# Optimization experiments

Hardware: AMD Instinct MI355X
Metric: run time of the kernel (lower is better)

Reference implementation:

```python
import jax, jax.numpy as jnp
import numpy as np

B, N, DI, DS, DP, DM, S = 64, 4096, 64, 64, 64, 128, 7
NUM_ITER = 3
EPS_ATTN = 1e-8
LN_EPS = 1e-5


def setup_inputs() -> dict:
    key = jax.random.key(0)
    ks = jax.random.split(key, 12)
    rn = lambda k, shp, sc=1.0: (jax.random.normal(k, shp, jnp.float32) * sc)
    return {
        "x": rn(ks[0], (B, N, DI)),
        "ln_inp_g": jnp.ones((DI,), jnp.float32),
        "ln_inp_b": jnp.zeros((DI,), jnp.float32),
        "ln_slot_g": jnp.ones((DS,), jnp.float32),
        "ln_slot_b": jnp.zeros((DS,), jnp.float32),
        "slots_init": rn(ks[1], (1, S, DS)),
        "Wk": rn(ks[2], (DI, DP), 1.0 / np.sqrt(DI)),
        "Wv": rn(ks[3], (DI, DP), 1.0 / np.sqrt(DI)),
        "Wq": rn(ks[4], (DS, DP), 1.0 / np.sqrt(DS)),
        "gru_wih": rn(ks[5], (3 * DS, DP), 1.0 / np.sqrt(DS)),
        "gru_whh": rn(ks[6], (3 * DS, DS), 1.0 / np.sqrt(DS)),
        "gru_bih": jnp.zeros((3 * DS,), jnp.float32),
        "gru_bhh": jnp.zeros((3 * DS,), jnp.float32),
        "mlp_w1": rn(ks[7], (DS, DM), 1.0 / np.sqrt(DS)),
        "mlp_b1": jnp.zeros((DM,), jnp.float32),
        "mlp_w2": rn(ks[8], (DM, DS), 1.0 / np.sqrt(DM)),
        "mlp_b2": jnp.zeros((DS,), jnp.float32),
    }


def _layernorm(x, g, b):
    m = jnp.mean(x, axis=-1, keepdims=True)
    v = jnp.mean(jnp.square(x - m), axis=-1, keepdims=True)
    return (x - m) * jax.lax.rsqrt(v + LN_EPS) * g + b


def _gru_cell(u, h, wih, whh, bih, bhh):
    # PyTorch GRUCell semantics
    gi = u @ wih.T + bih  # [*, 3*DS]
    gh = h @ whh.T + bhh
    ir, iz, inn = jnp.split(gi, 3, axis=-1)
    hr, hz, hn = jnp.split(gh, 3, axis=-1)
    r = jax.nn.sigmoid(ir + hr)
    z = jax.nn.sigmoid(iz + hz)
    n = jnp.tanh(inn + r * hn)
    return (1.0 - z) * n + z * h


def reference(x, ln_inp_g, ln_inp_b, ln_slot_g, ln_slot_b, slots_init,
              Wk, Wv, Wq, gru_wih, gru_whh, gru_bih, gru_bhh,
              mlp_w1, mlp_b1, mlp_w2, mlp_b2):
    x = _layernorm(x, ln_inp_g, ln_inp_b)          # [B,N,DI]
    k = x @ Wk                                      # [B,N,DP] (hoisted; x fixed across iters)
    v = x @ Wv                                      # [B,N,DP]
    slots = jnp.broadcast_to(slots_init, (x.shape[0], S, DS))
    scale = 1.0 / np.sqrt(DP)
    for _ in range(NUM_ITER):
        slots_prev = slots
        sn = _layernorm(slots, ln_slot_g, ln_slot_b)
        q = sn @ Wq                                 # [B,S,DP]
        attn = jnp.einsum('bnd,bsd->bns', k, q) * scale
        attn = jax.nn.softmax(attn, axis=-1) + EPS_ATTN      # softmax over slots
        weights = attn / jnp.sum(attn, axis=1, keepdims=True)  # normalize over N
        updates = jnp.einsum('bns,bnd->bsd', weights, v)     # [B,S,DP]
        h = _gru_cell(updates.reshape(-1, DP), slots_prev.reshape(-1, DS),
                      gru_wih, gru_whh, gru_bih, gru_bhh)
        slots = h.reshape(-1, S, DS)
        slots = slots + (jax.nn.relu(slots @ mlp_w1 + mlp_b1) @ mlp_w2 + mlp_b2)
    return slots
```

## Files before the change

kernel.cpp:

```cpp
#include <hip/hip_runtime.h>
#include <stdint.h>

#define L2E 1.44269504088896f

static __device__ __forceinline__ float wsum(float v) {
    #pragma unroll
    for (int m = 1; m < 64; m <<= 1) v += __shfl_xor(v, m, 64);
    return v;
}
static __device__ __forceinline__ float sigm(float x) {
    return 1.0f / (1.0f + __builtin_amdgcn_exp2f(-x * L2E));
}
static __device__ __forceinline__ float tanh_(float x) {
    const float ax = fabsf(x);
    const float t = __builtin_amdgcn_exp2f(-2.0f * ax * L2E);
    const float r = (1.0f - t) / (1.0f + t);
    return (x < 0.f) ? -r : r;
}

template <int CTRL>
static __device__ __forceinline__ float dppterm(float v) {
    return __int_as_float(__builtin_amdgcn_update_dpp(
        0, __float_as_int(v), CTRL, 0xF, 0xF, true));
}
static __device__ __forceinline__ float red8(float v) {
    v += dppterm<0xB1>(v);
    v += dppterm<0x4E>(v);
    v += dppterm<0x141>(v);
    return v;
}

__global__ __launch_bounds__(256) void init_kernel(
    const float* __restrict__ s0,
    const float* __restrict__ lsg, const float* __restrict__ lsb,
    const float* __restrict__ Wq,  const float* __restrict__ Wk,
    const float* __restrict__ lig, const float* __restrict__ lib,
    const float* __restrict__ wih, const float* __restrict__ whh,
    float* __restrict__ slots, float* __restrict__ gkq, float* __restrict__ aux,
    float* __restrict__ wihT, float* __restrict__ whhT, float* __restrict__ WkT)
{
    __shared__ float wkT[4096];
    __shared__ float scr[4][64];
    const int tid = threadIdx.x, lane = tid & 63, wv = tid >> 6;
    const int idx = blockIdx.x * 256 + tid;

    if (idx < 12288) {
        const int i = idx / 192, j = idx - i * 192;
        wihT[idx] = wih[j * 64 + i];
    } else if (idx < 24576) {
        const int o = idx - 12288;
        const int i = o / 192, j = o - i * 192;
        whhT[o] = whh[j * 64 + i];
    } else {
        const int o = idx - 24576;
        const int p = o >> 6, d = o & 63;
        WkT[o] = Wk[d * 64 + p];
    }

    const int r = blockIdx.x * 4 + wv;
    const int s = r % 7;
    #pragma unroll
    for (int i = tid; i < 4096; i += 256) {
        const int d = i >> 6, p = i & 63;
        wkT[p * 64 + d] = Wk[i];
    }
    const float h = s0[s * 64 + lane];
    slots[r * 64 + lane] = h;
    __syncthreads();

    const float mean = wsum(h) * (1.0f / 64.0f);
    const float d = h - mean;
    const float var = wsum(d * d) * (1.0f / 64.0f);
    const float rs = rsqrtf(var + 1e-5f);
    const float sn = d * rs * lsg[lane] + lsb[lane];
    scr[wv][lane] = sn;
    __syncthreads();
    float q = 0.f;
    #pragma unroll 8
    for (int i = 0; i < 64; ++i) q = fmaf(scr[wv][i], Wq[i * 64 + lane], q);
    q *= 0.125f;
    __syncthreads();
    scr[wv][lane] = q;
    __syncthreads();
    float kq = 0.f;
    #pragma unroll 8
    for (int p = 0; p < 64; ++p) kq = fmaf(wkT[p * 64 + lane], scr[wv][p], kq);
    const float bk = wsum(lib[lane] * kq);
    const float gk = lig[lane] * kq;
    const float g1 = wsum(gk);
    gkq[r * 64 + lane] = gk;
    if (lane == 0) { aux[r * 2] = g1; aux[r * 2 + 1] = bk; }
}

__global__ __launch_bounds__(256, 2) void attn_kernel(
    const float* __restrict__ x,
    const float* __restrict__ gkq, const float* __restrict__ aux,
    float* __restrict__ Ypart)
{
    __shared__ float ybuf[16][460];
    const int tid = threadIdx.x, lane = tid & 63, wv = tid >> 6;
    const int b = blockIdx.x >> 4, chunk16 = blockIdx.x & 15;
    const int ck  = lane & 7;
    const int rsl = lane >> 3;

    float gk[7][8];
    {
        const float4* gp = (const float4*)(gkq + b * 448 + ck * 8);
        #pragma unroll
        for (int s = 0; s < 7; ++s) {
            const float4 u0 = gp[s * 16], u1 = gp[s * 16 + 1];
            gk[s][0] = u0.x; gk[s][1] = u0.y; gk[s][2] = u0.z; gk[s][3] = u0.w;
            gk[s][4] = u1.x; gk[s][5] = u1.y; gk[s][6] = u1.z; gk[s][7] = u1.w;
        }
    }
    const float* ab = aux + b * 14;
    float g1[7], bk[7];
    #pragma unroll
    for (int s = 0; s < 7; ++s) { g1[s] = ab[2 * s]; bk[s] = ab[2 * s + 1]; }

    float Yacc[7][8];
    #pragma unroll
    for (int s = 0; s < 7; ++s)
        #pragma unroll
        for (int j = 0; j < 8; ++j) Yacc[s][j] = 0.f;
    float cacc[7] = {0.f, 0.f, 0.f, 0.f, 0.f, 0.f, 0.f};

    const float* rb = x + (((long)b * 4096) + chunk16 * 256 + wv * 64 + rsl) * 64
                        + ck * 8;
    float4 a0 = *(const float4*)(rb);
    float4 a1 = *(const float4*)(rb + 4);
    #pragma unroll 1
    for (int g = 0; g < 8; ++g) {
        const int gn = (g < 7) ? g + 1 : 7;
        const float4 b0 = *(const float4*)(rb + gn * 512);
        const float4 b1 = *(const float4*)(rb + gn * 512 + 4);

        const float xv[8] = {a0.x, a0.y, a0.z, a0.w, a1.x, a1.y, a1.z, a1.w};
        float sum = 0.f, ss = 0.f;
        #pragma unroll
        for (int j = 0; j < 8; ++j) { sum += xv[j]; ss = fmaf(xv[j], xv[j], ss); }
        float acc[7];
        #pragma unroll
        for (int s = 0; s < 7; ++s) {
            float a = 0.f;
            #pragma unroll
            for (int j = 0; j < 8; ++j) a = fmaf(xv[j], gk[s][j], a);
            acc[s] = a;
        }
        sum = red8(sum);
        ss  = red8(ss);
        #pragma unroll
        for (int s = 0; s < 7; ++s) acc[s] = red8(acc[s]);

        const float m   = sum * (1.0f / 64.0f);
        const float var = ss * (1.0f / 64.0f) - m * m;
        const float rs  = rsqrtf(var + 1e-5f);
        const float rsm = rs * m;
        float t[7];
        #pragma unroll
        for (int s = 0; s < 7; ++s)
            t[s] = fmaf(rs, acc[s], fmaf(-rsm, g1[s], bk[s]));
        float mx = t[0];
        #pragma unroll
        for (int s = 1; s < 7; ++s) mx = fmaxf(mx, t[s]);
        float e[7], se = 0.f;
        #pragma unroll
        for (int s = 0; s < 7; ++s) {
            e[s] = __builtin_amdgcn_exp2f((t[s] - mx) * L2E);
            se += e[s];
        }
        const float inv = 1.0f / se;
        #pragma unroll
        for (int s = 0; s < 7; ++s) {
            const float w = fmaf(e[s], inv, 1e-8f);
            cacc[s] += w;
            const float wrs = w * rs;
            #pragma unroll
            for (int j = 0; j < 8; ++j)
                Yacc[s][j] = fmaf(wrs, xv[j], Yacc[s][j]);
        }
        a0 = b0; a1 = b1;
    }

    #pragma unroll
    for (int s = 0; s < 7; ++s) {
        #pragma unroll
        for (int j = 0; j < 8; ++j)
            Yacc[s][j] += dppterm<0x128>(Yacc[s][j]);
        cacc[s] += dppterm<0x128>(cacc[s]);
    }
    if (((lane >> 3) & 1) == 0) {
        const int sub = lane >> 4;
        float* yb = &ybuf[wv * 4 + sub][ck * 8];
        #pragma unroll
        for (int s = 0; s < 7; ++s) {
            #pragma unroll
            for (int j = 0; j < 8; ++j) yb[s * 64 + j] = Yacc[s][j];
        }
        if (ck == 0) {
            #pragma unroll
            for (int s = 0; s < 7; ++s)
                ybuf[wv * 4 + sub][448 + s] = cacc[s];
        }
    }
    __syncthreads();
    for (int i = tid; i < 455; i += 256) {
        float v = 0.f;
        #pragma unroll
        for (int p = 0; p < 16; ++p) v += ybuf[p][i];
        Ypart[((long)b * 16 + chunk16) * 456 + i] = v;
    }
}

__global__ __launch_bounds__(512) void update_kernel(
    const float* __restrict__ Ypart, float* __restrict__ slots,
    const float* __restrict__ Wv,
    const float* __restrict__ wihT, const float* __restrict__ whhT,
    const float* __restrict__ bih,  const float* __restrict__ bhh,
    const float* __restrict__ w1,   const float* __restrict__ b1,
    const float* __restrict__ w2,   const float* __restrict__ b2,
    const float* __restrict__ lsg,  const float* __restrict__ lsb,
    const float* __restrict__ Wq,   const float* __restrict__ WkT,
    const float* __restrict__ lig,  const float* __restrict__ lib,
    float* __restrict__ gkq, float* __restrict__ aux,
    float* __restrict__ out, int last)
{
    __shared__ float wsYd[7][64];
    __shared__ float wsC[8];
    __shared__ float wss[7][4][64];
    const int tid = threadIdx.x, lane = tid & 63, wv = tid >> 6;
    const int b = blockIdx.x;
    const float* Yb = Ypart + (long)b * 16 * 456;

    if (tid < 448) {
        float v = 0.f;
        #pragma unroll
        for (int c = 0; c < 16; ++c) v += Yb[c * 456 + tid];
        wsYd[tid >> 6][tid & 63] = v;
    } else if (tid < 455) {
        const int s = tid - 448;
        float v = 0.f;
        #pragma unroll
        for (int c = 0; c < 16; ++c) v += Yb[c * 456 + 448 + s];
        wsC[s] = v;
    }
    __syncthreads();

    if (wv < 7) {
        const int s = wv;
        const int r = b * 7 + s;
        float (*scr)[64] = wss[wv];

        const float Yd = wsYd[s][lane];
        const float C  = wsC[s];
        const float Z  = wsum(Yd) * (1.0f / 64.0f);
        const float a  = (lig[lane] * (Yd - Z) + lib[lane] * C) / C;
        scr[0][lane] = a;
        float u = 0.f;
        #pragma unroll 8
        for (int i = 0; i < 64; ++i) u = fmaf(scr[0][i], Wv[i * 64 + lane], u);
        const float h = slots[r * 64 + lane];
        scr[1][lane] = u;
        scr[2][lane] = h;

        float gi0 = bih[lane], gi1 = bih[64 + lane], gi2 = bih[128 + lane];
        float gh0 = bhh[lane], gh1 = bhh[64 + lane], gh2 = bhh[128 + lane];
        #pragma unroll 4
        for (int i = 0; i < 64; ++i) {
            const float ui = scr[1][i], hi = scr[2][i];
            const float* wi = &wihT[i * 192];
            const float* wh = &whhT[i * 192];
            gi0 = fmaf(ui, wi[lane], gi0);
            gi1 = fmaf(ui, wi[64 + lane], gi1);
            gi2 = fmaf(ui, wi[128 + lane], gi2);
            gh0 = fmaf(hi, wh[lane], gh0);
            gh1 = fmaf(hi, wh[64 + lane], gh1);
            gh2 = fmaf(hi, wh[128 + lane], gh2);
        }
        const float rr = sigm(gi0 + gh0);
        const float zz = sigm(gi1 + gh1);
        const float nn = tanh_(gi2 + rr * gh2);
        const float hn = (1.f - zz) * nn + zz * h;
        scr[0][lane] = hn;

        float m0 = b1[lane], m1 = b1[64 + lane];
        #pragma unroll 8
        for (int i = 0; i < 64; ++i) {
            const float hi = scr[0][i];
            m0 = fmaf(hi, w1[i * 128 + lane], m0);
            m1 = fmaf(hi, w1[i * 128 + 64 + lane], m1);
        }
        scr[1][lane] = fmaxf(m0, 0.f);
        scr[2][lane] = fmaxf(m1, 0.f);

        float o2 = b2[lane];
        #pragma unroll 8
        for (int t = 0; t < 64; ++t)
            o2 = fmaf(scr[1][t], w2[t * 64 + lane], o2);
        #pragma unroll 8
        for (int t = 0; t < 64; ++t)
            o2 = fmaf(scr[2][t], w2[(64 + t) * 64 + lane], o2);
        const float snv = hn + o2;
        slots[r * 64 + lane] = snv;
        if (last) {
            out[r * 64 + lane] = snv;
        } else {
            const float mean = wsum(snv) * (1.0f / 64.0f);
            const float d = snv - mean;
            const float var = wsum(d * d) * (1.0f / 64.0f);
            const float rs = rsqrtf(var + 1e-5f);
            const float sn = d * rs * lsg[lane] + lsb[lane];
            scr[3][lane] = sn;
            float q = 0.f;
            #pragma unroll 8
            for (int i = 0; i < 64; ++i) q = fmaf(scr[3][i], Wq[i * 64 + lane], q);
            q *= 0.125f;
            scr[0][lane] = q;
            float kq = 0.f;
            #pragma unroll 8
            for (int p = 0; p < 64; ++p) kq = fmaf(WkT[p * 64 + lane], scr[0][p], kq);
            const float bk2 = wsum(lib[lane] * kq);
            const float gkv = lig[lane] * kq;
            const float g1v = wsum(gkv);
            gkq[r * 64 + lane] = gkv;
            if (lane == 0) { aux[r * 2] = g1v; aux[r * 2 + 1] = bk2; }
        }
    }
}

extern "C" void kernel_launch(void* const* d_in, const int* in_sizes, int n_in,
                              void* d_out, int out_size, void* d_ws, size_t ws_size,
                              hipStream_t stream)
{
    const float* x   = (const float*)d_in[0];
    const float* lig = (const float*)d_in[1];
    const float* lib = (const float*)d_in[2];
    const float* lsg = (const float*)d_in[3];
    const float* lsb = (const float*)d_in[4];
    const float* s0  = (const float*)d_in[5];
    const float* Wk  = (const float*)d_in[6];
    const float* Wv  = (const float*)d_in[7];
    const float* Wq  = (const float*)d_in[8];
    const float* wih = (const float*)d_in[9];
    const float* whh = (const float*)d_in[10];
    const float* bih = (const float*)d_in[11];
    const float* bhh = (const float*)d_in[12];
    const float* w1  = (const float*)d_in[13];
    const float* b1  = (const float*)d_in[14];
    const float* w2  = (const float*)d_in[15];
    const float* b2  = (const float*)d_in[16];

    float* f = (float*)d_ws;
    float* gkq   = f; f += 448 * 64;
    float* aux   = f; f += 448 * 2;
    float* slots = f; f += 448 * 64;
    float* Ypart = f; f += (long)64 * 16 * 456;
    float* wihT  = f; f += 64 * 192;
    float* whhT  = f; f += 64 * 192;
    float* WkT   = f; f += 64 * 64;

    init_kernel<<<112, 256, 0, stream>>>(s0, lsg, lsb, Wq, Wk, lig, lib,
                                         wih, whh, slots, gkq, aux,
                                         wihT, whhT, WkT);
    for (int it = 0; it < 3; ++it) {
        attn_kernel<<<1024, 256, 0, stream>>>(x, gkq, aux, Ypart);
        update_kernel<<<64, 512, 0, stream>>>(
            Ypart, slots, Wv, wihT, whhT, bih, bhh, w1, b1, w2, b2,
            lsg, lsb, Wq, WkT, lig, lib, gkq, aux,
            (float*)d_out, it == 2);
    }
}
```

Baseline: 240.4 us.

## Stage x tiles into LDS via async loads and cache update weights in LDS

The attention kernel now uses global_load_lds to copy each 8-row x tile straight into a per-wave double-buffered LDS array, with explicit vmcnt waits and a fully unrolled eight-step schedule, replacing the register prefetch loop. The goal is to keep more loads in flight and hide global latency behind the softmax work. The update kernel now first copies Wv, the GRU weights and the first MLP weight matrix into shared memory (about 147 KB) before the matvecs. That trades repeated global reads for a large upfront copy and heavy LDS use, which can cap occupancy at one block per CU.

```diff
diff --git a/kernel.cpp b/kernel.cpp
--- a/kernel.cpp
+++ b/kernel.cpp
@@ -92,12 +92,88 @@
     if (lane == 0) { aux[r * 2] = g1; aux[r * 2 + 1] = bk; }
 }
 
+#define PROC(A0, A1)                                                         \
+    do {                                                                     \
+        const float xv[8] = {A0.x, A0.y, A0.z, A0.w, A1.x, A1.y, A1.z, A1.w};\
+        float sum = 0.f, ss = 0.f;                                           \
+        _Pragma("unroll")                                                    \
+        for (int j = 0; j < 8; ++j) {                                        \
+            sum += xv[j]; ss = fmaf(xv[j], xv[j], ss);                       \
+        }                                                                    \
+        float acc[7];                                                        \
+        _Pragma("unroll")                                                    \
+        for (int s = 0; s < 7; ++s) {                                        \
+            float a = 0.f;                                                   \
+            _Pragma("unroll")                                                \
+            for (int j = 0; j < 8; ++j) a = fmaf(xv[j], gk[s][j], a);        \
+            acc[s] = a;                                                      \
+        }                                                                    \
+        sum = red8(sum);                                                     \
+        ss  = red8(ss);                                                      \
+        _Pragma("unroll")                                                    \
+        for (int s = 0; s < 7; ++s) acc[s] = red8(acc[s]);                   \
+        const float m   = sum * (1.0f / 64.0f);                              \
+        const float var = ss * (1.0f / 64.0f) - m * m;                       \
+        const float rs  = rsqrtf(var + 1e-5f);                               \
+        const float rsm = rs * m;                                            \
+        float t[7];                                                          \
+        _Pragma("unroll")                                                    \
+        for (int s = 0; s < 7; ++s)                                          \
+            t[s] = fmaf(rs, acc[s], fmaf(-rsm, g1[s], bk[s]));               \
+        float mx = t[0];                                                     \
+        _Pragma("unroll")                                                    \
+        for (int s = 1; s < 7; ++s) mx = fmaxf(mx, t[s]);                    \
+        float e[7], se = 0.f;                                                \
+        _Pragma("unroll")                                                    \
+        for (int s = 0; s < 7; ++s) {                                        \
+            e[s] = __builtin_amdgcn_exp2f((t[s] - mx) * L2E);                \
+            se += e[s];                                                      \
+        }                                                                    \
+        const float inv = 1.0f / se;                                         \
+        _Pragma("unroll")                                                    \
+        for (int s = 0; s < 7; ++s) {                                        \
+            const float w = fmaf(e[s], inv, 1e-8f);                          \
+            cacc[s] += w;                                                    \
+            const float wrs = w * rs;                                        \
+            _Pragma("unroll")                                                \
+            for (int j = 0; j < 8; ++j)                                      \
+                Yacc[s][j] = fmaf(wrs, xv[j], Yacc[s][j]);                   \
+        }                                                                    \
+    } while (0)
+
+#define STAGE(G, BUF)                                                        \
+    do {                                                                     \
+        const char* gs_ = (const char*)xw + (G) * 2048 + lane * 16;          \
+        char* ls_ = (char*)&xbuf[wv][BUF][0][0];                             \
+        __builtin_amdgcn_global_load_lds(                                    \
+            (const __attribute__((address_space(1))) unsigned int*)gs_,      \
+            (__attribute__((address_space(3))) unsigned int*)ls_, 16, 0, 0); \
+        __builtin_amdgcn_global_load_lds(                                    \
+            (const __attribute__((address_space(1))) unsigned int*)(gs_ + 1024), \
+            (__attribute__((address_space(3))) unsigned int*)(ls_ + 1024),   \
+            16, 0, 0);                                                       \
+    } while (0)
+
+#define WAITV(N)                                                             \
+    do {                                                                     \
+        asm volatile("s_waitcnt vmcnt(" #N ")" ::: "memory");                \
+        __builtin_amdgcn_sched_barrier(0);                                   \
+    } while (0)
+
+#define PROCL(BUF)                                                           \
+    do {                                                                     \
+        const float4 A0_ = *(const float4*)&xbuf[wv][BUF][rsl][ck * 8];      \
+        const float4 A1_ = *(const float4*)&xbuf[wv][BUF][rsl][ck * 8 + 4];  \
+        PROC(A0_, A1_);                                                      \
+    } while (0)
+
 __global__ __launch_bounds__(256, 2) void attn_kernel(
     const float* __restrict__ x,
     const float* __restrict__ gkq, const float* __restrict__ aux,
     float* __restrict__ Ypart)
 {
     __shared__ float ybuf[16][460];
+    __shared__ float xbuf[4][2][8][64];
     const int tid = threadIdx.x, lane = tid & 63, wv = tid >> 6;
     const int b = blockIdx.x >> 4, chunk16 = blockIdx.x & 15;
     const int ck  = lane & 7;
@@ -125,62 +201,20 @@
         for (int j = 0; j < 8; ++j) Yacc[s][j] = 0.f;
     float cacc[7] = {0.f, 0.f, 0.f, 0.f, 0.f, 0.f, 0.f};
 
-    const float* rb = x + (((long)b * 4096) + chunk16 * 256 + wv * 64 + rsl) * 64
-                        + ck * 8;
-    float4 a0 = *(const float4*)(rb);
-    float4 a1 = *(const float4*)(rb + 4);
-    #pragma unroll 1
-    for (int g = 0; g < 8; ++g) {
-        const int gn = (g < 7) ? g + 1 : 7;
-        const float4 b0 = *(const float4*)(rb + gn * 512);
-        const float4 b1 = *(const float4*)(rb + gn * 512 + 4);
-
-        const float xv[8] = {a0.x, a0.y, a0.z, a0.w, a1.x, a1.y, a1.z, a1.w};
-        float sum = 0.f, ss = 0.f;
-        #pragma unroll
-        for (int j = 0; j < 8; ++j) { sum += xv[j]; ss = fmaf(xv[j], xv[j], ss); }
-        float acc[7];
-        #pragma unroll
-        for (int s = 0; s < 7; ++s) {
-            float a = 0.f;
-            #pragma unroll
-            for (int j = 0; j < 8; ++j) a = fmaf(xv[j], gk[s][j], a);
-            acc[s] = a;
-        }
-        sum = red8(sum);
-        ss  = red8(ss);
-        #pragma unroll
-        for (int s = 0; s < 7; ++s) acc[s] = red8(acc[s]);
-
-        const float m   = sum * (1.0f / 64.0f);
-        const float var = ss * (1.0f / 64.0f) - m * m;
-        const float rs  = rsqrtf(var + 1e-5f);
-        const float rsm = rs * m;
-        float t[7];
-        #pragma unroll
-        for (int s = 0; s < 7; ++s)
-            t[s] = fmaf(rs, acc[s], fmaf(-rsm, g1[s], bk[s]));
-        float mx = t[0];
-        #pragma unroll
-        for (int s = 1; s < 7; ++s) mx = fmaxf(mx, t[s]);
-        float e[7], se = 0.f;
-        #pragma unroll
-        for (int s = 0; s < 7; ++s) {
-            e[s] = __builtin_amdgcn_exp2f((t[s] - mx) * L2E);
-            se += e[s];
-        }
-        const float inv = 1.0f / se;
-        #pragma unroll
-        for (int s = 0; s < 7; ++s) {
-            const float w = fmaf(e[s], inv, 1e-8f);
-            cacc[s] += w;
-            const float wrs = w * rs;
-            #pragma unroll
-            for (int j = 0; j < 8; ++j)
-                Yacc[s][j] = fmaf(wrs, xv[j], Yacc[s][j]);
-        }
-        a0 = b0; a1 = b1;
-    }
+    const float* xw = x + (((long)b * 4096) + chunk16 * 256 + wv * 64) * 64;
+
+    asm volatile("s_waitcnt vmcnt(0)" ::: "memory");
+    __builtin_amdgcn_sched_barrier(0);
+
+    STAGE(0, 0);
+    STAGE(1, 1); WAITV(2); PROCL(0);
+    STAGE(2, 0); WAITV(2); PROCL(1);
+    STAGE(3, 1); WAITV(2); PROCL(0);
+    STAGE(4, 0); WAITV(2); PROCL(1);
+    STAGE(5, 1); WAITV(2); PROCL(0);
+    STAGE(6, 0); WAITV(2); PROCL(1);
+    STAGE(7, 1); WAITV(2); PROCL(0);
+                 WAITV(0); PROCL(1);
 
     #pragma unroll
     for (int s = 0; s < 7; ++s) {
@@ -225,12 +259,35 @@
     float* __restrict__ gkq, float* __restrict__ aux,
     float* __restrict__ out, int last)
 {
+    __shared__ float lWv[4096];
+    __shared__ float lwih[12288];
+    __shared__ float lwhh[12288];
+    __shared__ float lw1[8192];
     __shared__ float wsYd[7][64];
     __shared__ float wsC[8];
     __shared__ float wss[7][4][64];
     const int tid = threadIdx.x, lane = tid & 63, wv = tid >> 6;
     const int b = blockIdx.x;
     const float* Yb = Ypart + (long)b * 16 * 456;
+
+    {
+        const float4* g0 = (const float4*)Wv;
+        float4*       s0 = (float4*)lWv;
+        #pragma unroll
+        for (int i = 0; i < 2; ++i) s0[tid + i * 512] = g0[tid + i * 512];
+        const float4* g1 = (const float4*)wihT;
+        float4*       s1 = (float4*)lwih;
+        #pragma unroll
+        for (int i = 0; i < 6; ++i) s1[tid + i * 512] = g1[tid + i * 512];
+        const float4* g2 = (const float4*)whhT;
+        float4*       s2 = (float4*)lwhh;
+        #pragma unroll
+        for (int i = 0; i < 6; ++i) s2[tid + i * 512] = g2[tid + i * 512];
+        const float4* g3 = (const float4*)w1;
+        float4*       s3 = (float4*)lw1;
+        #pragma unroll
+        for (int i = 0; i < 4; ++i) s3[tid + i * 512] = g3[tid + i * 512];
+    }
 
     if (tid < 448) {
         float v = 0.f;
@@ -258,7 +315,7 @@
         scr[0][lane] = a;
         float u = 0.f;
         #pragma unroll 8
-        for (int i = 0; i < 64; ++i) u = fmaf(scr[0][i], Wv[i * 64 + lane], u);
+        for (int i = 0; i < 64; ++i) u = fmaf(scr[0][i], lWv[i * 64 + lane], u);
         const float h = slots[r * 64 + lane];
         scr[1][lane] = u;
         scr[2][lane] = h;
@@ -268,8 +325,8 @@
         #pragma unroll 4
         for (int i = 0; i < 64; ++i) {
             const float ui = scr[1][i], hi = scr[2][i];
-            const float* wi = &wihT[i * 192];
-            const float* wh = &whhT[i * 192];
+            const float* wi = &lwih[i * 192];
+            const float* wh = &lwhh[i * 192];
             gi0 = fmaf(ui, wi[lane], gi0);
             gi1 = fmaf(ui, wi[64 + lane], gi1);
             gi2 = fmaf(ui, wi[128 + lane], gi2);
@@ -287,8 +344,8 @@
         #pragma unroll 8
         for (int i = 0; i < 64; ++i) {
             const float hi = scr[0][i];
-            m0 = fmaf(hi, w1[i * 128 + lane], m0);
-            m1 = fmaf(hi, w1[i * 128 + 64 + lane], m1);
+            m0 = fmaf(hi, lw1[i * 128 + lane], m0);
+            m1 = fmaf(hi, lw1[i * 128 + 64 + lane], m1);
         }
         scr[1][lane] = fmaxf(m0, 0.f);
         scr[2][lane] = fmaxf(m1, 0.f);
```

Measured after the change: 225.6 us. 1.07x faster.
